# Kernel tuning notes

Measured on AMD Instinct MI355X. Metric: run time of the kernel, lower is better.

The kernel has to match this reference:

```python
import jax, jax.numpy as jnp
import numpy as np

SLOPE = 0.2

def setup_inputs() -> dict:
    key = jax.random.key(0)
    ks = jax.random.split(key, 24)
    B, O, M, Nb = 16, 1024, 64, 64
    in_ope, in_mas, in_arc, out = 16, 8, 8, 32
    f = lambda k, s: jax.random.normal(k, s, dtype=jnp.float32)
    adj = lambda k, s: jax.random.randint(k, s, 0, 2).astype(jnp.float32)
    return {
        'adj0': adj(ks[0], (O, M)),
        'adj1': adj(ks[1], (O, M)),
        'adj2': adj(ks[2], (O, Nb)),
        'adj3': adj(ks[3], (O, Nb)),
        'batch_idxes': jnp.arange(B, dtype=jnp.int64),
        'feat_opes': f(ks[4], (B, O, in_ope)),
        'feat_mas': f(ks[5], (B, M, in_mas)),
        'feat_buf': f(ks[6], (B, Nb, in_mas)),
        'feat_arc_ma_in': f(ks[7], (B, O, M, in_arc)),
        'feat_arc_buf_in': f(ks[8], (B, O, Nb, in_arc)),
        'feat_arc_ma_out': f(ks[9], (B, O, M, in_arc)),
        'feat_arc_buf_out': f(ks[10], (B, O, Nb, in_arc)),
        'W_ope': f(ks[11], (in_ope, out)) * 0.2,
        'W_mas': f(ks[12], (in_mas, out)) * 0.2,
        'W_buf': f(ks[13], (in_mas, out)) * 0.2,
        'W_arc_in': f(ks[14], (in_arc, out)) * 0.2,
        'W_arc_out': f(ks[15], (in_arc, out)) * 0.2,
        'attn_ope': jax.random.uniform(ks[16], (out,), dtype=jnp.float32),
        'attn_mas': jax.random.uniform(ks[17], (out,), dtype=jnp.float32),
        'attn_arc': jax.random.uniform(ks[18], (out,), dtype=jnp.float32),
    }

def _branch(adj_in, adj_out, p_ope, p_node, p_arc_in, p_arc_out, e_ope, e_node, e_arc_in, e_arc_out):
    # adj_*: [O,N]; e_ope: [B,O,1]; e_node: [B,N,1]; e_arc_*: [B,O,N,1]
    def scores(A2, e_arc):
        A = A2[None, :, :, None]                               # [1,O,N,1]
        a = A * e_ope[:, :, None, :] + e_arc + A * e_node[:, None, :, :]
        return jax.nn.leaky_relu(a, SLOPE)                     # [B,O,N,1]
    eik_in = scores(adj_in, e_arc_in)
    eik_out = scores(adj_out, e_arc_out)
    ekk = jax.nn.leaky_relu(e_node + e_node, SLOPE)            # [B,N,1]
    def alphas(A2, eik):
        e = jnp.concatenate([eik, ekk[:, None]], axis=1)       # [B,O+1,N,1]
        mask = jnp.concatenate([A2 == 1.0, jnp.ones((1, A2.shape[1]), dtype=bool)], axis=0)
        e = jnp.where(mask[None, :, :, None], e, -jnp.inf)
        return jax.nn.softmax(e[..., 0], axis=1)               # [B,O+1,N] over neighbors
    al_in = alphas(adj_in, eik_in)
    al_out = alphas(adj_out, eik_out)
    # NOTE: Wmu_out replicates the original's missing-parens expression exactly
    Wmu_in = jnp.sum((p_arc_in + p_ope[:, :, None, :]) * al_in[:, :-1, :, None], axis=1)   # [B,N,F]
    Wmu_out = jnp.sum(p_arc_out + p_ope[:, :, None, :] * al_out[:, :-1, :, None], axis=1)  # [B,N,F]
    Wmu_kk = p_node * (al_in[:, -1, :] + al_out[:, -1, :])[..., None]                      # [B,N,F]
    return jax.nn.sigmoid(Wmu_in + Wmu_out + Wmu_kk)

def reference(adj0, adj1, adj2, adj3, batch_idxes, feat_opes, feat_mas, feat_buf,
              feat_arc_ma_in, feat_arc_buf_in, feat_arc_ma_out, feat_arc_buf_out,
              W_ope, W_mas, W_buf, W_arc_in, W_arc_out, attn_ope, attn_mas, attn_arc):
    p_ope = feat_opes @ W_ope              # [B,O,F]
    p_mas = feat_mas @ W_mas               # [B,M,F]
    p_buf = feat_buf @ W_buf               # [B,Nb,F]
    p_arc_ma_in = feat_arc_ma_in @ W_arc_in
    p_arc_buf_in = feat_arc_buf_in @ W_arc_in
    p_arc_ma_out = feat_arc_ma_out @ W_arc_out
    p_arc_buf_out = feat_arc_buf_out @ W_arc_out
    score = lambda p, a: jnp.sum(p * a, axis=-1, keepdims=True)
    e_ope = score(p_ope, attn_ope)
    e_mas = score(p_mas, attn_mas)
    e_buf = score(p_buf, attn_mas)         # original uses attn_mas for buffers too
    nu_mas = _branch(adj0, adj1, p_ope, p_mas, p_arc_ma_in, p_arc_ma_out,
                     e_ope, e_mas, score(p_arc_ma_in, attn_arc), score(p_arc_ma_out, attn_arc))
    nu_buf = _branch(adj2, adj3, p_ope, p_buf, p_arc_buf_in, p_arc_buf_out,
                     e_ope, e_buf, score(p_arc_buf_in, attn_arc), score(p_arc_buf_out, attn_arc))
    return (nu_mas, nu_buf)
```

## Files before the change

### kernel.cpp

```cpp
#include <hip/hip_runtime.h>
#include <math.h>

#define B_   16
#define O_   1024
#define M_   64
#define C_   32
#define INO  16
#define INA  8
#define S_CH 32
#define SLOPE 0.2f

#define NF    50
#define NCOL  (2*B_*M_)

#define WS_EOPE   0
#define WS_ENODE  (WS_EOPE + B_*O_)
#define WS_PNODE  (WS_ENODE + 2*B_*M_)
#define WS_WARC   (WS_PNODE + 2*B_*M_*C_)
#define WS_ACC    (WS_WARC + 16)

__global__ void k_pre(const float* __restrict__ feat_opes,
                      const float* __restrict__ feat_mas,
                      const float* __restrict__ feat_buf,
                      const float* __restrict__ W_ope,
                      const float* __restrict__ W_mas,
                      const float* __restrict__ W_buf,
                      const float* __restrict__ W_arc_in,
                      const float* __restrict__ W_arc_out,
                      const float* __restrict__ attn_ope,
                      const float* __restrict__ attn_mas,
                      const float* __restrict__ attn_arc,
                      float* __restrict__ ws) {
    int tid = threadIdx.x;
    int bid = blockIdx.x;
    if (bid < 64) {
        __shared__ float wo[INO];
        if (tid < INO) {
            float s = 0.f;
            for (int c = 0; c < C_; ++c) s += W_ope[tid*C_ + c]*attn_ope[c];
            wo[tid] = s;
        }
        __syncthreads();
        int idx = bid*256 + tid;
        const float* f = feat_opes + idx*INO;
        float s = 0.f;
#pragma unroll
        for (int j = 0; j < INO; ++j) s += f[j]*wo[j];
        ws[WS_EOPE + idx] = s;
    } else if (bid < 72) {
        int idx = (bid - 64)*256 + tid;
        int br  = idx >> 10;
        int rem = idx & 1023;
        const float* f = (br == 0 ? feat_mas : feat_buf) + rem*INA;
        const float* W = (br == 0 ? W_mas : W_buf);
        float f8[INA];
#pragma unroll
        for (int k = 0; k < INA; ++k) f8[k] = f[k];
        float e = 0.f;
        float* pn = ws + WS_PNODE + idx*C_;
        for (int c = 0; c < C_; ++c) {
            float s = 0.f;
#pragma unroll
            for (int k = 0; k < INA; ++k) s += f8[k]*W[k*C_ + c];
            pn[c] = s;
            e += s*attn_mas[c];
        }
        ws[WS_ENODE + idx] = e;
    } else if (bid == 72) {
        if (tid < 16) {
            const float* W = (tid < 8) ? W_arc_in : W_arc_out;
            int k = tid & 7;
            float s = 0.f;
            for (int c = 0; c < C_; ++c) s += W[k*C_ + c]*attn_arc[c];
            ws[WS_WARC + tid] = s;
        }
    } else {
        int idx = (bid - 73)*256 + tid;
        ws[WS_ACC + idx] = 0.f;
    }
}

__global__ __launch_bounds__(256) void k_main(
        const float* __restrict__ adj0, const float* __restrict__ adj1,
        const float* __restrict__ adj2, const float* __restrict__ adj3,
        const float* __restrict__ feat_opes,
        const float* __restrict__ fin_ma,  const float* __restrict__ fin_buf,
        const float* __restrict__ fout_ma, const float* __restrict__ fout_buf,
        float* __restrict__ ws) {
    int tid = threadIdx.x;
    int m = tid & 63;
    int y = tid >> 6;
    int bid = blockIdx.x;
    int chunk = bid & (S_CH - 1);
    int t = bid >> 5;
    int b = t & (B_ - 1);
    int br = t >> 4;

    const float* A_in  = br ? adj2 : adj0;
    const float* A_out = br ? adj3 : adj1;
    const float* fin   = br ? fin_buf  : fin_ma;
    const float* fout  = br ? fout_buf : fout_ma;

    int o0 = chunk*32 + y*8;

    float e_node_m = ws[WS_ENODE + (br*B_ + b)*M_ + m];

    const float* wv = ws + WS_WARC;
    float w_in0=wv[0],w_in1=wv[1],w_in2=wv[2],w_in3=wv[3];
    float w_in4=wv[4],w_in5=wv[5],w_in6=wv[6],w_in7=wv[7];
    float w_ot0=wv[8],w_ot1=wv[9],w_ot2=wv[10],w_ot3=wv[11];
    float w_ot4=wv[12],w_ot5=wv[13],w_ot6=wv[14],w_ot7=wv[15];

    const float* e_ope = ws + WS_EOPE + b*O_ + o0;
    float eo[8];
#pragma unroll
    for (int i = 0; i < 8; ++i) eo[i] = e_ope[i];

    float aA[8], aB[8];
    const float* Ai = A_in  + o0*M_ + m;
    const float* Ao = A_out + o0*M_ + m;
#pragma unroll
    for (int i = 0; i < 8; ++i) { aA[i] = Ai[i*M_]; aB[i] = Ao[i*M_]; }

    const float* pi = fin  + ((size_t)(b*O_ + o0)*M_ + m)*INA;
    const float* po = fout + ((size_t)(b*O_ + o0)*M_ + m)*INA;
    const int OSTR = M_*INA;

    float ai[8], sao[8], wiv[8], wov[8];
#pragma unroll
    for (int k = 0; k < 8; ++k) { ai[k] = 0.f; sao[k] = 0.f; }

    float4 i0 = *(const float4*)(pi);
    float4 i1 = *(const float4*)(pi + 4);
    float4 u0 = *(const float4*)(po);
    float4 u1 = *(const float4*)(po + 4);

#pragma unroll
    for (int it = 0; it < 8; ++it) {
        float4 ni0, ni1, nu0, nu1;
        if (it < 7) {
            const float* qi = pi + (it+1)*OSTR;
            const float* qo = po + (it+1)*OSTR;
            ni0 = *(const float4*)(qi);
            ni1 = *(const float4*)(qi + 4);
            nu0 = *(const float4*)(qo);
            nu1 = *(const float4*)(qo + 4);
        }
        float ein = i0.x*w_in0 + i0.y*w_in1 + i0.z*w_in2 + i0.w*w_in3
                  + i1.x*w_in4 + i1.y*w_in5 + i1.z*w_in6 + i1.w*w_in7;
        float eut = u0.x*w_ot0 + u0.y*w_ot1 + u0.z*w_ot2 + u0.w*w_ot3
                  + u1.x*w_ot4 + u1.y*w_ot5 + u1.z*w_ot6 + u1.w*w_ot7;
        float base = eo[it] + e_node_m;
        float si = base + ein;  si = si > 0.f ? si : SLOPE*si;
        float so = base + eut;  so = so > 0.f ? so : SLOPE*so;
        float wi = (aA[it] == 1.0f) ? __expf(si) : 0.f;
        float wo_ = (aB[it] == 1.0f) ? __expf(so) : 0.f;
        wiv[it] = wi; wov[it] = wo_;
        ai[0] += wi*i0.x; ai[1] += wi*i0.y; ai[2] += wi*i0.z; ai[3] += wi*i0.w;
        ai[4] += wi*i1.x; ai[5] += wi*i1.y; ai[6] += wi*i1.z; ai[7] += wi*i1.w;
        sao[0] += u0.x; sao[1] += u0.y; sao[2] += u0.z; sao[3] += u0.w;
        sao[4] += u1.x; sao[5] += u1.y; sao[6] += u1.z; sao[7] += u1.w;
        i0 = ni0; i1 = ni1; u0 = nu0; u1 = nu1;
    }

    float l_in = 0.f, l_out = 0.f;
#pragma unroll
    for (int it = 0; it < 8; ++it) { l_in += wiv[it]; l_out += wov[it]; }

    float aoi[16], aoo[16];
#pragma unroll
    for (int j = 0; j < 16; ++j) { aoi[j] = 0.f; aoo[j] = 0.f; }
    const float* fo_base = feat_opes + (size_t)(b*O_ + o0)*INO;
#pragma unroll
    for (int it = 0; it < 8; ++it) {
        const float4* fp = (const float4*)(fo_base + it*INO);
        float4 f0 = fp[0], f1 = fp[1], f2 = fp[2], f3 = fp[3];
        float wi = wiv[it], wo_ = wov[it];
        aoi[0]  += wi*f0.x; aoi[1]  += wi*f0.y; aoi[2]  += wi*f0.z; aoi[3]  += wi*f0.w;
        aoi[4]  += wi*f1.x; aoi[5]  += wi*f1.y; aoi[6]  += wi*f1.z; aoi[7]  += wi*f1.w;
        aoi[8]  += wi*f2.x; aoi[9]  += wi*f2.y; aoi[10] += wi*f2.z; aoi[11] += wi*f2.w;
        aoi[12] += wi*f3.x; aoi[13] += wi*f3.y; aoi[14] += wi*f3.z; aoi[15] += wi*f3.w;
        aoo[0]  += wo_*f0.x; aoo[1]  += wo_*f0.y; aoo[2]  += wo_*f0.z; aoo[3]  += wo_*f0.w;
        aoo[4]  += wo_*f1.x; aoo[5]  += wo_*f1.y; aoo[6]  += wo_*f1.z; aoo[7]  += wo_*f1.w;
        aoo[8]  += wo_*f2.x; aoo[9]  += wo_*f2.y; aoo[10] += wo_*f2.z; aoo[11] += wo_*f2.w;
        aoo[12] += wo_*f3.x; aoo[13] += wo_*f3.y; aoo[14] += wo_*f3.z; aoo[15] += wo_*f3.w;
    }

    float v[NF];
    v[0] = l_in;
#pragma unroll
    for (int k = 0; k < 8; ++k)  v[1+k]  = ai[k];
#pragma unroll
    for (int j = 0; j < 16; ++j) v[9+j]  = aoi[j];
    v[25] = l_out;
#pragma unroll
    for (int j = 0; j < 16; ++j) v[26+j] = aoo[j];
#pragma unroll
    for (int k = 0; k < 8; ++k)  v[42+k] = sao[k];

    __shared__ float red[3][NF][64];
    if (y > 0) {
#pragma unroll
        for (int f = 0; f < NF; ++f) red[y-1][f][m] = v[f];
    }
    __syncthreads();
    if (y == 0) {
#pragma unroll
        for (int f = 0; f < NF; ++f)
            v[f] += red[0][f][m] + red[1][f][m] + red[2][f][m];
        float* acc = ws + WS_ACC;
        int col = (br*B_ + b)*M_ + m;
#pragma unroll
        for (int f = 0; f < NF; ++f)
            unsafeAtomicAdd(acc + f*NCOL + col, v[f]);
    }
}

__global__ __launch_bounds__(64) void k_fin(
        const float* __restrict__ W_ope,
        const float* __restrict__ W_arc_in,
        const float* __restrict__ W_arc_out,
        const float* __restrict__ ws,
        float* __restrict__ out) {
    int m = threadIdx.x;
    int bid = blockIdx.x;
    int b  = bid & (B_ - 1);
    int br = bid >> 4;
    int col = (br*B_ + b)*M_ + m;

    __shared__ float sW[1024];
    for (int i = m; i < 512; i += 64) sW[i] = W_ope[i];
    for (int i = m; i < 256; i += 64) { sW[512 + i] = W_arc_in[i]; sW[768 + i] = W_arc_out[i]; }
    __syncthreads();

    const float* acc = ws + WS_ACC;
    float v[NF];
#pragma unroll
    for (int f = 0; f < NF; ++f) v[f] = acc[f*NCOL + col];

    const float* pn = ws + WS_PNODE + col*C_;
    float pc[C_];
#pragma unroll
    for (int q = 0; q < 8; ++q) {
        float4 p4 = *(const float4*)(pn + 4*q);
        pc[4*q] = p4.x; pc[4*q+1] = p4.y; pc[4*q+2] = p4.z; pc[4*q+3] = p4.w;
    }

    float en  = ws[WS_ENODE + col];
    float ekk = 2.f*en; ekk = ekk > 0.f ? ekk : SLOPE*ekk;
    float wkk = __expf(ekk);

    float inv_i = 1.f / (v[0]  + wkk);
    float inv_o = 1.f / (v[25] + wkk);
    float akk   = wkk*inv_i + wkk*inv_o;

    float* op = out + (size_t)col*C_;
#pragma unroll 4
    for (int c = 0; c < C_; ++c) {
        float s_ai = 0.f, s_oi = 0.f, s_ao = 0.f, s_oo = 0.f;
#pragma unroll
        for (int k = 0; k < 8; ++k) {
            s_ai += v[1+k] *sW[512 + k*C_ + c];
            s_ao += v[42+k]*sW[768 + k*C_ + c];
        }
#pragma unroll
        for (int j = 0; j < 16; ++j) {
            float wv = sW[j*C_ + c];
            s_oi += v[9+j]*wv;
            s_oo += v[26+j]*wv;
        }
        float x = (s_ai + s_oi)*inv_i + s_ao + s_oo*inv_o + pc[c]*akk;
        op[c] = 1.f/(1.f + __expf(-x));
    }
}

extern "C" void kernel_launch(void* const* d_in, const int* in_sizes, int n_in,
                              void* d_out, int out_size, void* d_ws, size_t ws_size,
                              hipStream_t stream) {
    const float* adj0 = (const float*)d_in[0];
    const float* adj1 = (const float*)d_in[1];
    const float* adj2 = (const float*)d_in[2];
    const float* adj3 = (const float*)d_in[3];
    const float* feat_opes       = (const float*)d_in[5];
    const float* feat_mas        = (const float*)d_in[6];
    const float* feat_buf        = (const float*)d_in[7];
    const float* feat_arc_ma_in  = (const float*)d_in[8];
    const float* feat_arc_buf_in = (const float*)d_in[9];
    const float* feat_arc_ma_out = (const float*)d_in[10];
    const float* feat_arc_buf_out= (const float*)d_in[11];
    const float* W_ope    = (const float*)d_in[12];
    const float* W_mas    = (const float*)d_in[13];
    const float* W_buf    = (const float*)d_in[14];
    const float* W_arc_in = (const float*)d_in[15];
    const float* W_arc_out= (const float*)d_in[16];
    const float* attn_ope = (const float*)d_in[17];
    const float* attn_mas = (const float*)d_in[18];
    const float* attn_arc = (const float*)d_in[19];

    float* ws  = (float*)d_ws;
    float* out = (float*)d_out;

    k_pre<<<473, 256, 0, stream>>>(feat_opes, feat_mas, feat_buf,
                                   W_ope, W_mas, W_buf, W_arc_in, W_arc_out,
                                   attn_ope, attn_mas, attn_arc, ws);

    k_main<<<2*B_*S_CH, 256, 0, stream>>>(adj0, adj1, adj2, adj3, feat_opes,
                                          feat_arc_ma_in, feat_arc_buf_in,
                                          feat_arc_ma_out, feat_arc_buf_out, ws);

    k_fin<<<2*B_, 64, 0, stream>>>(W_ope, W_arc_in, W_arc_out, ws, out);
}
```

Before: 210.9 us.

## Split in/out arc streams across separate warps with 512-thread blocks

The main kernel now runs 512 threads per block. Waves 0-3 handle the incoming-arc stream and waves 4-7 handle the outgoing-arc stream, instead of each thread processing both. This halves per-thread register state and doubles the number of in-flight threads, which should help latency hiding on the memory-bound arc-feature reads. The accumulator layout is reordered: the out-part sum of arc features moves ahead of its feat_opes sums, and the finish kernel is updated to the new indices. The explicit software prefetch was dropped, and feat_opes is now read by both halves.

```diff
diff --git a/kernel.cpp b/kernel.cpp
--- a/kernel.cpp
+++ b/kernel.cpp
@@ -7,10 +7,10 @@
 #define C_   32
 #define INO  16
 #define INA  8
-#define S_CH 32
 #define SLOPE 0.2f
 
 #define NF    50
+#define NFH   25
 #define NCOL  (2*B_*M_)
 
 #define WS_EOPE   0
@@ -80,139 +80,103 @@
     }
 }
 
-__global__ __launch_bounds__(256) void k_main(
+__global__ __launch_bounds__(512, 6) void k_main(
         const float* __restrict__ adj0, const float* __restrict__ adj1,
         const float* __restrict__ adj2, const float* __restrict__ adj3,
         const float* __restrict__ feat_opes,
         const float* __restrict__ fin_ma,  const float* __restrict__ fin_buf,
         const float* __restrict__ fout_ma, const float* __restrict__ fout_buf,
-        float* __restrict__ ws) {
+        const float* __restrict__ ws_ro,
+        float* __restrict__ acc) {
     int tid = threadIdx.x;
-    int m = tid & 63;
-    int y = tid >> 6;
+    int m  = tid & 63;
+    int w  = tid >> 6;
+    int wl = w & 3;
+    bool isOut = (w >= 4);
     int bid = blockIdx.x;
-    int chunk = bid & (S_CH - 1);
+    int chunk = bid & 31;
     int t = bid >> 5;
-    int b = t & (B_ - 1);
+    int b  = t & (B_ - 1);
     int br = t >> 4;
-
-    const float* A_in  = br ? adj2 : adj0;
-    const float* A_out = br ? adj3 : adj1;
-    const float* fin   = br ? fin_buf  : fin_ma;
-    const float* fout  = br ? fout_buf : fout_ma;
-
-    int o0 = chunk*32 + y*8;
-
-    float e_node_m = ws[WS_ENODE + (br*B_ + b)*M_ + m];
-
-    const float* wv = ws + WS_WARC;
-    float w_in0=wv[0],w_in1=wv[1],w_in2=wv[2],w_in3=wv[3];
-    float w_in4=wv[4],w_in5=wv[5],w_in6=wv[6],w_in7=wv[7];
-    float w_ot0=wv[8],w_ot1=wv[9],w_ot2=wv[10],w_ot3=wv[11];
-    float w_ot4=wv[12],w_ot5=wv[13],w_ot6=wv[14],w_ot7=wv[15];
-
-    const float* e_ope = ws + WS_EOPE + b*O_ + o0;
+    int o0 = chunk*32 + wl*8;
+
+    const float* A = isOut ? (br ? adj3 : adj1) : (br ? adj2 : adj0);
+    const float* F = isOut ? (br ? fout_buf : fout_ma) : (br ? fin_buf : fin_ma);
+
+    const float* wvp = ws_ro + WS_WARC + (isOut ? 8 : 0);
+    float w0=wvp[0],w1=wvp[1],w2=wvp[2],w3=wvp[3];
+    float w4=wvp[4],w5=wvp[5],w6=wvp[6],w7=wvp[7];
+
+    float e_node_m = ws_ro[WS_ENODE + (br*B_ + b)*M_ + m];
+
+    const float* eop = ws_ro + WS_EOPE + b*O_ + o0;
     float eo[8];
 #pragma unroll
-    for (int i = 0; i < 8; ++i) eo[i] = e_ope[i];
-
-    float aA[8], aB[8];
-    const float* Ai = A_in  + o0*M_ + m;
-    const float* Ao = A_out + o0*M_ + m;
-#pragma unroll
-    for (int i = 0; i < 8; ++i) { aA[i] = Ai[i*M_]; aB[i] = Ao[i*M_]; }
-
-    const float* pi = fin  + ((size_t)(b*O_ + o0)*M_ + m)*INA;
-    const float* po = fout + ((size_t)(b*O_ + o0)*M_ + m)*INA;
+    for (int i = 0; i < 8; ++i) eo[i] = eop[i];
+
+    const float* Ap = A + o0*M_ + m;
+    float av[8];
+#pragma unroll
+    for (int i = 0; i < 8; ++i) av[i] = Ap[i*M_];
+
+    const float* P = F + ((size_t)(b*O_ + o0)*M_ + m)*INA;
     const int OSTR = M_*INA;
 
-    float ai[8], sao[8], wiv[8], wov[8];
-#pragma unroll
-    for (int k = 0; k < 8; ++k) { ai[k] = 0.f; sao[k] = 0.f; }
-
-    float4 i0 = *(const float4*)(pi);
-    float4 i1 = *(const float4*)(pi + 4);
-    float4 u0 = *(const float4*)(po);
-    float4 u1 = *(const float4*)(po + 4);
+    const float* fo = feat_opes + (size_t)(b*O_ + o0)*INO;
+
+    float acc_l = 0.f;
+    float a8[8];
+    float a16[16];
+#pragma unroll
+    for (int k = 0; k < 8; ++k)  a8[k] = 0.f;
+#pragma unroll
+    for (int j = 0; j < 16; ++j) a16[j] = 0.f;
 
 #pragma unroll
     for (int it = 0; it < 8; ++it) {
-        float4 ni0, ni1, nu0, nu1;
-        if (it < 7) {
-            const float* qi = pi + (it+1)*OSTR;
-            const float* qo = po + (it+1)*OSTR;
-            ni0 = *(const float4*)(qi);
-            ni1 = *(const float4*)(qi + 4);
-            nu0 = *(const float4*)(qo);
-            nu1 = *(const float4*)(qo + 4);
-        }
-        float ein = i0.x*w_in0 + i0.y*w_in1 + i0.z*w_in2 + i0.w*w_in3
-                  + i1.x*w_in4 + i1.y*w_in5 + i1.z*w_in6 + i1.w*w_in7;
-        float eut = u0.x*w_ot0 + u0.y*w_ot1 + u0.z*w_ot2 + u0.w*w_ot3
-                  + u1.x*w_ot4 + u1.y*w_ot5 + u1.z*w_ot6 + u1.w*w_ot7;
-        float base = eo[it] + e_node_m;
-        float si = base + ein;  si = si > 0.f ? si : SLOPE*si;
-        float so = base + eut;  so = so > 0.f ? so : SLOPE*so;
-        float wi = (aA[it] == 1.0f) ? __expf(si) : 0.f;
-        float wo_ = (aB[it] == 1.0f) ? __expf(so) : 0.f;
-        wiv[it] = wi; wov[it] = wo_;
-        ai[0] += wi*i0.x; ai[1] += wi*i0.y; ai[2] += wi*i0.z; ai[3] += wi*i0.w;
-        ai[4] += wi*i1.x; ai[5] += wi*i1.y; ai[6] += wi*i1.z; ai[7] += wi*i1.w;
-        sao[0] += u0.x; sao[1] += u0.y; sao[2] += u0.z; sao[3] += u0.w;
-        sao[4] += u1.x; sao[5] += u1.y; sao[6] += u1.z; sao[7] += u1.w;
-        i0 = ni0; i1 = ni1; u0 = nu0; u1 = nu1;
-    }
-
-    float l_in = 0.f, l_out = 0.f;
-#pragma unroll
-    for (int it = 0; it < 8; ++it) { l_in += wiv[it]; l_out += wov[it]; }
-
-    float aoi[16], aoo[16];
-#pragma unroll
-    for (int j = 0; j < 16; ++j) { aoi[j] = 0.f; aoo[j] = 0.f; }
-    const float* fo_base = feat_opes + (size_t)(b*O_ + o0)*INO;
-#pragma unroll
-    for (int it = 0; it < 8; ++it) {
-        const float4* fp = (const float4*)(fo_base + it*INO);
-        float4 f0 = fp[0], f1 = fp[1], f2 = fp[2], f3 = fp[3];
-        float wi = wiv[it], wo_ = wov[it];
-        aoi[0]  += wi*f0.x; aoi[1]  += wi*f0.y; aoi[2]  += wi*f0.z; aoi[3]  += wi*f0.w;
-        aoi[4]  += wi*f1.x; aoi[5]  += wi*f1.y; aoi[6]  += wi*f1.z; aoi[7]  += wi*f1.w;
-        aoi[8]  += wi*f2.x; aoi[9]  += wi*f2.y; aoi[10] += wi*f2.z; aoi[11] += wi*f2.w;
-        aoi[12] += wi*f3.x; aoi[13] += wi*f3.y; aoi[14] += wi*f3.z; aoi[15] += wi*f3.w;
-        aoo[0]  += wo_*f0.x; aoo[1]  += wo_*f0.y; aoo[2]  += wo_*f0.z; aoo[3]  += wo_*f0.w;
-        aoo[4]  += wo_*f1.x; aoo[5]  += wo_*f1.y; aoo[6]  += wo_*f1.z; aoo[7]  += wo_*f1.w;
-        aoo[8]  += wo_*f2.x; aoo[9]  += wo_*f2.y; aoo[10] += wo_*f2.z; aoo[11] += wo_*f2.w;
-        aoo[12] += wo_*f3.x; aoo[13] += wo_*f3.y; aoo[14] += wo_*f3.z; aoo[15] += wo_*f3.w;
-    }
-
-    float v[NF];
-    v[0] = l_in;
-#pragma unroll
-    for (int k = 0; k < 8; ++k)  v[1+k]  = ai[k];
-#pragma unroll
-    for (int j = 0; j < 16; ++j) v[9+j]  = aoi[j];
-    v[25] = l_out;
-#pragma unroll
-    for (int j = 0; j < 16; ++j) v[26+j] = aoo[j];
-#pragma unroll
-    for (int k = 0; k < 8; ++k)  v[42+k] = sao[k];
-
-    __shared__ float red[3][NF][64];
-    if (y > 0) {
-#pragma unroll
-        for (int f = 0; f < NF; ++f) red[y-1][f][m] = v[f];
+        float4 x0 = *(const float4*)(P + it*OSTR);
+        float4 x1 = *(const float4*)(P + it*OSTR + 4);
+        float d = x0.x*w0 + x0.y*w1 + x0.z*w2 + x0.w*w3
+                + x1.x*w4 + x1.y*w5 + x1.z*w6 + x1.w*w7;
+        float s = eo[it] + e_node_m + d;
+        s = s > 0.f ? s : SLOPE*s;
+        float we = (av[it] == 1.0f) ? __expf(s) : 0.f;
+        acc_l += we;
+        if (isOut) {
+            a8[0] += x0.x; a8[1] += x0.y; a8[2] += x0.z; a8[3] += x0.w;
+            a8[4] += x1.x; a8[5] += x1.y; a8[6] += x1.z; a8[7] += x1.w;
+        } else {
+            a8[0] += we*x0.x; a8[1] += we*x0.y; a8[2] += we*x0.z; a8[3] += we*x0.w;
+            a8[4] += we*x1.x; a8[5] += we*x1.y; a8[6] += we*x1.z; a8[7] += we*x1.w;
+        }
+        const float* fr = fo + it*INO;
+#pragma unroll
+        for (int j = 0; j < 16; ++j) a16[j] += we*fr[j];
+    }
+
+    float v[NFH];
+    v[0] = acc_l;
+#pragma unroll
+    for (int k = 0; k < 8; ++k)  v[1+k] = a8[k];
+#pragma unroll
+    for (int j = 0; j < 16; ++j) v[9+j] = a16[j];
+
+    __shared__ float red[2][3][NFH][64];
+    int part = isOut ? 1 : 0;
+    if (wl > 0) {
+#pragma unroll
+        for (int f = 0; f < NFH; ++f) red[part][wl-1][f][m] = v[f];
     }
     __syncthreads();
-    if (y == 0) {
-#pragma unroll
-        for (int f = 0; f < NF; ++f)
-            v[f] += red[0][f][m] + red[1][f][m] + red[2][f][m];
-        float* acc = ws + WS_ACC;
+    if (wl == 0) {
+#pragma unroll
+        for (int f = 0; f < NFH; ++f)
+            v[f] += red[part][0][f][m] + red[part][1][f][m] + red[part][2][f][m];
         int col = (br*B_ + b)*M_ + m;
-#pragma unroll
-        for (int f = 0; f < NF; ++f)
-            unsafeAtomicAdd(acc + f*NCOL + col, v[f]);
+        int fb  = isOut ? NFH : 0;
+#pragma unroll
+        for (int f = 0; f < NFH; ++f)
+            unsafeAtomicAdd(acc + (fb + f)*NCOL + col, v[f]);
     }
 }
 
@@ -261,13 +225,13 @@
 #pragma unroll
         for (int k = 0; k < 8; ++k) {
             s_ai += v[1+k] *sW[512 + k*C_ + c];
-            s_ao += v[42+k]*sW[768 + k*C_ + c];
+            s_ao += v[26+k]*sW[768 + k*C_ + c];
         }
 #pragma unroll
         for (int j = 0; j < 16; ++j) {
             float wv = sW[j*C_ + c];
-            s_oi += v[9+j]*wv;
-            s_oo += v[26+j]*wv;
+            s_oi += v[9+j] *wv;
+            s_oo += v[34+j]*wv;
         }
         float x = (s_ai + s_oi)*inv_i + s_ao + s_oo*inv_o + pc[c]*akk;
         op[c] = 1.f/(1.f + __expf(-x));
@@ -304,9 +268,10 @@
                                    W_ope, W_mas, W_buf, W_arc_in, W_arc_out,
                                    attn_ope, attn_mas, attn_arc, ws);
 
-    k_main<<<2*B_*S_CH, 256, 0, stream>>>(adj0, adj1, adj2, adj3, feat_opes,
-                                          feat_arc_ma_in, feat_arc_buf_in,
-                                          feat_arc_ma_out, feat_arc_buf_out, ws);
+    k_main<<<2*B_*32, 512, 0, stream>>>(adj0, adj1, adj2, adj3, feat_opes,
+                                        feat_arc_ma_in, feat_arc_buf_in,
+                                        feat_arc_ma_out, feat_arc_buf_out,
+                                        ws, ws + WS_ACC);
 
     k_fin<<<2*B_, 64, 0, stream>>>(W_ope, W_arc_in, W_arc_out, ws, out);
 }
```

Measured after the change: 327.2 us. +55.2%, slower.
